# Performance work log

Hardware: AMD Instinct MI355X
Metric: run time of the kernel (lower is better)

The kernel has to match this reference:

```python
import math
import jax, jax.numpy as jnp
import numpy as np


def _sinkhorn_attn(q, n):
    """Log-domain Sinkhorn-Knopp, eps=1, max_iter=1, uniform marginals.
    cost C = -q @ q^T, so M = (-C + u + v)/eps = S + u + v with S = q q^T.
    Returns transport plan pi = exp(S + u_i + v_j).  q: [B, n, d]."""
    S = jnp.einsum('bnd,bmd->bnm', q, q)            # [B, n, n]
    log_marg = -math.log(n)                          # log(1/n)
    u = log_marg - jax.nn.logsumexp(S, axis=-1)      # [B, n] row update
    v = log_marg - jax.nn.logsumexp(S + u[..., :, None], axis=-2)  # [B, n] col update
    return jnp.exp(S + u[..., :, None] + v[..., None, :])


def reference(x, row_embed, col_embed):
    # x: [B, d, H, W]; row_embed/col_embed: [len_embedding, d//2]
    B, d, H, W = x.shape
    # learned positional embedding: [H, W, d] -> [d, H, W]
    x_emb = col_embed[:W]                             # [W, F]
    y_emb = row_embed[:H]                             # [H, F]
    F = x_emb.shape[-1]
    pos = jnp.concatenate([
        jnp.broadcast_to(x_emb[None, :, :], (H, W, F)),
        jnp.broadcast_to(y_emb[:, None, :], (H, W, F)),
    ], axis=-1).transpose(2, 0, 1)                    # [d, H, W]
    x = x + pos[None]

    n = H * W
    xf = x.reshape(B, d, n).transpose(0, 2, 1)        # [B, n, d] = q = k = v (v unscaled)
    inv_sqrtV = 1.0 / math.sqrt(math.sqrt(d))         # d**-0.25 applied to q and k each
    attn = _sinkhorn_attn(xf * inv_sqrtV, n)          # [B, n, n]
    out = jnp.einsum('bnm,bmd->bnd', attn, xf)        # [B, n, d]
    return out.transpose(0, 2, 1).reshape(B, d, H, W)


def setup_inputs() -> dict:
    key = jax.random.key(0)
    k1, k2, k3 = jax.random.split(key, 3)
    B, d, H, W = 32, 512, 32, 32
    len_emb, F = 32, d // 2
    return {
        'x': jax.random.normal(k1, (B, d, H, W), dtype=jnp.float32),
        'row_embed': jax.random.uniform(k2, (len_emb, F), dtype=jnp.float32),
        'col_embed': jax.random.uniform(k3, (len_emb, F), dtype=jnp.float32),
    }
```

## Files before the change

kernel.cpp:

```cpp
#include <hip/hip_runtime.h>
#include <hip/hip_fp16.h>
#include <math.h>

typedef _Float16 f16;
typedef _Float16 f16x8 __attribute__((ext_vector_type(8)));
typedef _Float16 f16x4 __attribute__((ext_vector_type(4)));
typedef float f32x4 __attribute__((ext_vector_type(4)));

namespace {
constexpr int kB = 32, kD = 512, kN = 1024, kF = 256;
constexpr float kScale = 0.04419417382415922f;
constexpr float kLogMarg = -6.931471805599453f;
constexpr float kPInv = 1.f / 16384.f;
}

__device__ __forceinline__ void gload16(const void* g, void* l) {
  __builtin_amdgcn_global_load_lds(
      (const __attribute__((address_space(1))) void*)g,
      (__attribute__((address_space(3))) void*)l, 16, 0, 0);
}

__global__ __launch_bounds__(256) void k_prep(
    const float* __restrict__ x, const float* __restrict__ re,
    const float* __restrict__ ce, f16* __restrict__ xf,
    f16* __restrict__ xfT, int b0) {
  __shared__ f16 T[64][68];
  const int lb = blockIdx.z;
  const int i0 = blockIdx.x * 64, c0 = blockIdx.y * 64;
  const int t = threadIdx.x;
  const int il = (t & 15) * 4;
  const int cl = t >> 4;
  const size_t xbase = ((size_t)(b0 + lb) * kD) * kN;
#pragma unroll
  for (int p = 0; p < 4; p++) {
    const int c = c0 + cl + 16 * p;
    const int i = i0 + il;
    const float4 xv = *(const float4*)(x + xbase + (size_t)c * kN + i);
    float4 pv;
    if (c < kF) {
      pv.x = ce[((i + 0) & 31) * kF + c];
      pv.y = ce[((i + 1) & 31) * kF + c];
      pv.z = ce[((i + 2) & 31) * kF + c];
      pv.w = ce[((i + 3) & 31) * kF + c];
    } else {
      const float r = re[(i >> 5) * kF + (c - kF)];
      pv.x = r; pv.y = r; pv.z = r; pv.w = r;
    }
    const f16 h0 = (f16)(xv.x + pv.x), h1 = (f16)(xv.y + pv.y);
    const f16 h2 = (f16)(xv.z + pv.z), h3 = (f16)(xv.w + pv.w);
    f16* dT = xfT + ((size_t)lb * kD + c) * kN + i;
    *(f16x4*)dT = (f16x4){h0, h1, h2, h3};
    T[cl + 16 * p][il + 0] = h0; T[cl + 16 * p][il + 1] = h1;
    T[cl + 16 * p][il + 2] = h2; T[cl + 16 * p][il + 3] = h3;
  }
  __syncthreads();
#pragma unroll
  for (int p = 0; p < 4; p++) {
    const int ir = cl + 16 * p;
    const int cc = il;
    const f16 h0 = T[cc + 0][ir], h1 = T[cc + 1][ir];
    const f16 h2 = T[cc + 2][ir], h3 = T[cc + 3][ir];
    f16* dF = xf + ((size_t)lb * kN + i0 + ir) * kD + c0 + cc;
    *(f16x4*)dF = (f16x4){h0, h1, h2, h3};
  }
}

__global__ __launch_bounds__(256) void k_gemm_s(
    const f16* __restrict__ xf, f16* __restrict__ S16,
    float* __restrict__ rp) {
  __shared__ char sm[65536];
  const int nwg = (int)(gridDim.x * gridDim.y * gridDim.z);
  const int lin = (int)(blockIdx.x +
                        gridDim.x * (blockIdx.y + gridDim.y * blockIdx.z));
  const int wid = (lin & 7) * (nwg >> 3) + (lin >> 3);
  const int bx = wid & 7, by = (wid >> 3) & 7, bz = wid >> 6;

  const int lb = bz;
  const int i0 = by * 128, j0 = bx * 128;
  const char* base = (const char*)(xf + (size_t)lb * kN * kD);
  const int t = threadIdx.x;
  const int w = t >> 6, lane = t & 63;
  const int m_off = (w >> 1) * 64, n_off = (w & 1) * 64;
  const int quad = lane >> 4, l15 = lane & 15;
  const int swz = (l15 & 7) << 4;

  int srcA[4], srcB[4], ldsw[4];
#pragma unroll
  for (int p = 0; p < 4; p++) {
    const int off = p * 4096 + w * 1024 + lane * 16;
    const int r = off >> 7;
    const int cb = (off & 127) ^ ((r & 7) << 4);
    srcA[p] = (i0 + r) * (kD * 2) + cb;
    srcB[p] = (j0 + r) * (kD * 2) + cb;
    ldsw[p] = p * 4096 + w * 1024;
  }

  f32x4 acc[4][4];
#pragma unroll
  for (int a = 0; a < 4; a++)
#pragma unroll
    for (int b = 0; b < 4; b++) acc[a][b] = (f32x4){0.f, 0.f, 0.f, 0.f};

#pragma unroll
  for (int p = 0; p < 4; p++) gload16(base + srcA[p], sm + ldsw[p]);
#pragma unroll
  for (int p = 0; p < 4; p++) gload16(base + srcB[p], sm + 16384 + ldsw[p]);
  __syncthreads();

#pragma unroll
  for (int tt = 0; tt < 8; tt++) {
    const int cur = tt & 1, nxt = cur ^ 1;
    if (tt + 1 < 8) {
      const int k0b = (tt + 1) * 128;
#pragma unroll
      for (int p = 0; p < 4; p++)
        gload16(base + srcA[p] + k0b, sm + (nxt << 15) + ldsw[p]);
#pragma unroll
      for (int p = 0; p < 4; p++)
        gload16(base + srcB[p] + k0b, sm + (nxt << 15) + 16384 + ldsw[p]);
    }
    const char* bA = sm + (cur << 15);
    const char* bB = bA + 16384;
#pragma unroll
    for (int kk = 0; kk < 2; kk++) {
      f16x8 af[4], bf[4];
#pragma unroll
      for (int q = 0; q < 4; q++)
        af[q] = *(const f16x8*)(bA + (m_off + 16 * q + l15) * 128 +
                                ((kk * 64 + quad * 16) ^ swz));
#pragma unroll
      for (int q = 0; q < 4; q++)
        bf[q] = *(const f16x8*)(bB + (n_off + 16 * q + l15) * 128 +
                                ((kk * 64 + quad * 16) ^ swz));
#pragma unroll
      for (int qa = 0; qa < 4; qa++)
#pragma unroll
        for (int qb = 0; qb < 4; qb++)
          acc[qa][qb] = __builtin_amdgcn_mfma_f32_16x16x32_f16(
              af[qa], bf[qb], acc[qa][qb], 0, 0, 0);
    }
    __syncthreads();
  }

  f16* Sb = S16 + (size_t)lb * kN * kN;
  const int jt2 = bx * 2 + (w & 1);
  float* rpb = rp + ((size_t)lb * 16 + jt2) * kN + i0 + m_off;
#pragma unroll
  for (int qa = 0; qa < 4; qa++) {
    const int i = i0 + m_off + 16 * qa + quad * 4;
    float rs[4] = {0.f, 0.f, 0.f, 0.f};
#pragma unroll
    for (int qb = 0; qb < 4; qb++) {
      const int j = j0 + n_off + 16 * qb + l15;
#pragma unroll
      for (int r = 0; r < 4; r++) {
        const f16 h = (f16)(acc[qa][qb][r] * kScale);
        Sb[(size_t)(i + r) * kN + j] = h;
        rs[r] += __expf((float)h);
      }
    }
#pragma unroll
    for (int r = 0; r < 4; r++) {
      float s = rs[r];
      s += __shfl_xor(s, 1);
      s += __shfl_xor(s, 2);
      s += __shfl_xor(s, 4);
      s += __shfl_xor(s, 8);
      if (l15 == 0) rpb[16 * qa + 4 * quad + r] = s;
    }
  }
}

__global__ __launch_bounds__(256) void k_u(
    const float* __restrict__ rp, float* __restrict__ u) {
  const int lb = blockIdx.y;
  const int i = blockIdx.x * 256 + threadIdx.x;
  const float* r = rp + (size_t)lb * 16 * kN + i;
  float s = 0.f;
#pragma unroll
  for (int t = 0; t < 16; t++) s += r[(size_t)t * kN];
  u[lb * kN + i] = kLogMarg - __logf(s);
}

__global__ __launch_bounds__(256) void k_cs(
    const f16* __restrict__ S16, const float* __restrict__ u,
    float* __restrict__ cp) {
  const int lb = blockIdx.z;
  const int seg = blockIdx.y;
  const int j = threadIdx.x * 4;
  const f16* Sb = S16 + (size_t)lb * kN * kN + (size_t)(seg * 64) * kN + j;
  const float* ub = u + lb * kN + seg * 64;
  float s0 = 0.f, s1 = 0.f, s2 = 0.f, s3 = 0.f;
#pragma unroll 8
  for (int r = 0; r < 64; r++) {
    const f16x4 v = *(const f16x4*)(Sb + (size_t)r * kN);
    const float ur = ub[r];
    s0 += __expf((float)v[0] + ur);
    s1 += __expf((float)v[1] + ur);
    s2 += __expf((float)v[2] + ur);
    s3 += __expf((float)v[3] + ur);
  }
  float4 o = {s0, s1, s2, s3};
  *(float4*)(cp + ((size_t)lb * 16 + seg) * kN + j) = o;
}

__global__ __launch_bounds__(256) void k_v(
    const float* __restrict__ cp, float* __restrict__ evp) {
  const int lb = blockIdx.y;
  const int j = blockIdx.x * 256 + threadIdx.x;
  const float* c = cp + (size_t)lb * 16 * kN + j;
  float s = 0.f;
#pragma unroll
  for (int r = 0; r < 16; r++) s += c[(size_t)r * kN];
  evp[lb * kN + j] = 16.f / s;
}

#define AF_READ(q)                                                          \
  _Pragma("unroll")                                                         \
  for (int pa = 0; pa < 2; pa++)                                            \
    _Pragma("unroll")                                                       \
    for (int kk = 0; kk < 2; kk++)                                          \
      af[pa][kk] = *(const f16x8*)(bA + (m_off + 32*(q) + 16*pa + l15)*128  \
                                   + ((kk*64 + quad*16) ^ swz));

#define MFMA_PH(q)                                                          \
  __builtin_amdgcn_s_setprio(1);                                            \
  _Pragma("unroll")                                                         \
  for (int pa = 0; pa < 2; pa++)                                            \
    _Pragma("unroll")                                                       \
    for (int qb = 0; qb < 4; qb++)                                          \
      _Pragma("unroll")                                                     \
      for (int kk = 0; kk < 2; kk++)                                        \
        acc[2*(q)+pa][qb] = __builtin_amdgcn_mfma_f32_16x16x32_f16(         \
            af[pa][kk], bf[qb][kk], acc[2*(q)+pa][qb], 0, 0, 0);            \
  __builtin_amdgcn_s_setprio(0);

__global__ __launch_bounds__(512) void k_gemm_o(
    const f16* __restrict__ xfT, const f16* __restrict__ S16,
    const float* __restrict__ u, const float* __restrict__ evp,
    float* __restrict__ out, int b0) {
  __shared__ char sm[135168];
  const int nwg = (int)(gridDim.x * gridDim.y * gridDim.z);
  const int lin = (int)(blockIdx.x +
                        gridDim.x * (blockIdx.y + gridDim.y * blockIdx.z));
  const int wid = (lin & 7) * (nwg >> 3) + (lin >> 3);
  const int bx = wid & 3, by = (wid >> 2) & 1, bz = wid >> 3;

  const int lb = bz;
  const int i0 = bx * 256, c0 = by * 256;
  const char* Ab = (const char*)(xfT + (size_t)lb * kD * kN);
  const char* Bb = (const char*)(S16 + (size_t)lb * kN * kN);
  const int t = threadIdx.x;
  const int w = t >> 6, lane = t & 63;
  const int wm = w >> 2, wn = w & 3;
  const int m_off = wm * 128, n_off = wn * 64;
  const int quad = lane >> 4, l15 = lane & 15;
  const int swz = (l15 & 7) << 4;

  int srcA[4], srcB[4], ldsw[4];
#pragma unroll
  for (int p = 0; p < 4; p++) {
    const int off = p * 8192 + t * 16;
    const int r = off >> 7;
    const int cb = (off & 127) ^ ((r & 7) << 4);
    srcA[p] = (c0 + r) * (kN * 2) + cb;
    srcB[p] = (i0 + r) * (kN * 2) + cb;
    ldsw[p] = p * 8192 + w * 1024;
  }

  float* evl = (float*)(sm + 131072);
  *(float2*)(evl + t * 2) = *(const float2*)(evp + (size_t)lb * kN + t * 2);
  float u4[4];
  const float* ub = u + (size_t)lb * kN + i0 + n_off + l15;
#pragma unroll
  for (int qb = 0; qb < 4; qb++) u4[qb] = ub[16 * qb];
  asm volatile("s_waitcnt vmcnt(0) lgkmcnt(0)" ::: "memory");
  __builtin_amdgcn_sched_barrier(0);

#pragma unroll
  for (int p = 0; p < 4; p++) gload16(Bb + srcB[p], sm + 65536 + ldsw[p]);
  gload16(Ab + srcA[0], sm + ldsw[0]);
  gload16(Ab + srcA[2], sm + ldsw[2]);
  gload16(Ab + srcA[1], sm + ldsw[1]);
  gload16(Ab + srcA[3], sm + ldsw[3]);
#pragma unroll
  for (int p = 0; p < 4; p++)
    gload16(Bb + srcB[p] + 128, sm + 65536 + 32768 + ldsw[p]);
  f32x4 acc[8][4];
#pragma unroll
  for (int a = 0; a < 8; a++)
#pragma unroll
    for (int b = 0; b < 4; b++) acc[a][b] = (f32x4){0.f, 0.f, 0.f, 0.f};
  asm volatile("s_waitcnt vmcnt(6)" ::: "memory");
  __builtin_amdgcn_s_barrier();
  __builtin_amdgcn_sched_barrier(0);

#pragma unroll
  for (int tt = 0; tt < 16; tt++) {
    const int cur = tt & 1, nxt = cur ^ 1;
    const char* bA = sm + cur * 32768;
    const char* bB = sm + 65536 + cur * 32768;
    char* wA = sm + nxt * 32768;
    char* wB = sm + 65536 + cur * 32768;
    const int kA = (tt + 1) * 128, kBB = (tt + 2) * 128;
    f16x8 bf[4][2], af[2][2];
    f16x8 raw[4][2];
#pragma unroll
    for (int qb = 0; qb < 4; qb++)
#pragma unroll
      for (int kk = 0; kk < 2; kk++)
        raw[qb][kk] = *(const f16x8*)(bB + (n_off + 16 * qb + l15) * 128 +
                                      ((kk * 64 + quad * 16) ^ swz));
    AF_READ(0)
    float4 e0[2], e1[2];
#pragma unroll
    for (int kk = 0; kk < 2; kk++) {
      const float* ep = evl + tt * 64 + kk * 32 + quad * 8;
      e0[kk] = *(const float4*)ep;
      e1[kk] = *(const float4*)(ep + 4);
    }
    asm volatile("s_waitcnt lgkmcnt(0)" ::: "memory");
    __builtin_amdgcn_sched_barrier(0);
    __builtin_amdgcn_s_barrier();
#pragma unroll
    for (int qb = 0; qb < 4; qb++)
#pragma unroll
      for (int kk = 0; kk < 2; kk++) {
        f16x8 o;
        o[0] = (f16)(__expf((float)raw[qb][kk][0] + u4[qb]) * e0[kk].x);
        o[1] = (f16)(__expf((float)raw[qb][kk][1] + u4[qb]) * e0[kk].y);
        o[2] = (f16)(__expf((float)raw[qb][kk][2] + u4[qb]) * e0[kk].z);
        o[3] = (f16)(__expf((float)raw[qb][kk][3] + u4[qb]) * e0[kk].w);
        o[4] = (f16)(__expf((float)raw[qb][kk][4] + u4[qb]) * e1[kk].x);
        o[5] = (f16)(__expf((float)raw[qb][kk][5] + u4[qb]) * e1[kk].y);
        o[6] = (f16)(__expf((float)raw[qb][kk][6] + u4[qb]) * e1[kk].z);
        o[7] = (f16)(__expf((float)raw[qb][kk][7] + u4[qb]) * e1[kk].w);
        bf[qb][kk] = o;
      }
    MFMA_PH(0)
    if (tt + 1 < 16) {
      gload16(Ab + srcA[0] + kA, wA + ldsw[0]);
      gload16(Ab + srcA[2] + kA, wA + ldsw[2]);
    }
    AF_READ(1)
    __builtin_amdgcn_s_barrier();
    MFMA_PH(1)
    if (tt == 15) { asm volatile("s_waitcnt vmcnt(0)" ::: "memory"); }
    else          { asm volatile("s_waitcnt vmcnt(6)" ::: "memory"); }
    __builtin_amdgcn_s_barrier();
    __builtin_amdgcn_sched_barrier(0);
    AF_READ(2)
    __builtin_amdgcn_s_barrier();
    MFMA_PH(2)
    if (tt + 1 < 16) {
      gload16(Ab + srcA[1] + kA, wA + ldsw[1]);
      gload16(Ab + srcA[3] + kA, wA + ldsw[3]);
    }
    if (tt + 2 < 16) {
#pragma unroll
      for (int p = 0; p < 4; p++)
        gload16(Bb + srcB[p] + kBB, wB + ldsw[p]);
    }
    AF_READ(3)
    __builtin_amdgcn_s_barrier();
    MFMA_PH(3)
    if (tt + 2 < 16)      { asm volatile("s_waitcnt vmcnt(6)" ::: "memory"); }
    else if (tt + 1 < 16) { asm volatile("s_waitcnt vmcnt(2)" ::: "memory"); }
    __builtin_amdgcn_s_barrier();
    __builtin_amdgcn_sched_barrier(0);
  }

  float* ob = out + ((size_t)(b0 + lb) * kD) * kN;
#pragma unroll
  for (int qa = 0; qa < 8; qa++) {
    const int c = c0 + m_off + 16 * qa + quad * 4;
#pragma unroll
    for (int qb = 0; qb < 4; qb++) {
      const int i = i0 + n_off + 16 * qb + l15;
#pragma unroll
      for (int r = 0; r < 4; r++)
        ob[(size_t)(c + r) * kN + i] = acc[qa][qb][r] * kPInv;
    }
  }
}

extern "C" void kernel_launch(void* const* d_in, const int* in_sizes, int n_in,
                              void* d_out, int out_size, void* d_ws, size_t ws_size,
                              hipStream_t stream) {
  const float* x = (const float*)d_in[0];
  const float* re = (const float*)d_in[1];
  const float* ce = (const float*)d_in[2];
  float* out = (float*)d_out;

  char* wsb = (char*)d_ws;
  const size_t perb = 2097152ull + 1048576 + 1048576 + 4096 + 4096 +
                      65536 + 65536;
  int G = (int)(ws_size / perb);
  if (G >= 32) G = 32;
  else if (G >= 16) G = 16;
  else if (G >= 8) G = 8;
  else if (G >= 4) G = 4;
  else if (G < 1) G = 1;
  f16* S16 = (f16*)wsb;
  f16* xf = (f16*)(wsb + (size_t)G * 2097152);
  f16* xfT = (f16*)((char*)xf + (size_t)G * 1048576);
  float* u = (float*)((char*)xfT + (size_t)G * 1048576);
  float* evp = u + (size_t)G * kN;
  float* rp = evp + (size_t)G * kN;
  float* cp = rp + (size_t)G * 16 * kN;

  for (int b0 = 0; b0 < kB; b0 += G) {
    const int g = (kB - b0 < G) ? (kB - b0) : G;
    k_prep<<<dim3(16, 8, g), 256, 0, stream>>>(x, re, ce, xf, xfT, b0);
    k_gemm_s<<<dim3(8, 8, g), 256, 0, stream>>>(xf, S16, rp);
    k_u<<<dim3(4, g), 256, 0, stream>>>(rp, u);
    k_cs<<<dim3(1, 16, g), 256, 0, stream>>>(S16, u, cp);
    k_v<<<dim3(4, g), 256, 0, stream>>>(cp, evp);
    k_gemm_o<<<dim3(4, 2, g), 512, 0, stream>>>(xfT, S16, u, evp, out, b0);
  }
}
```

Before: 257.9 us.

## Exploit symmetry of S in QK^T GEMM and precompute transport plan

Since S = q q^T is symmetric, the S GEMM now computes only the upper-triangular 128x128 tiles (36 per batch) and writes each off-diagonal tile's transpose, deriving the mirrored row-sum partials from column sums of the exponentials. A new elementwise kernel materializes the scaled transport plan exp(S+u+v) in fp16, so the output GEMM no longer does exp and scaling inside its inner loop. This roughly halves the MFMA work for S but adds strided transposed stores, an extra 2 MB per batch of workspace, and an extra read/write pass over the plan.

```diff
diff --git a/kernel.cpp b/kernel.cpp
--- a/kernel.cpp
+++ b/kernel.cpp
@@ -11,6 +11,8 @@
 constexpr int kB = 32, kD = 512, kN = 1024, kF = 256;
 constexpr float kScale = 0.04419417382415922f;
 constexpr float kLogMarg = -6.931471805599453f;
+constexpr float kMarg = 1.f / 1024.f;
+constexpr float kPScale = 16384.f;
 constexpr float kPInv = 1.f / 16384.f;
 }
 
@@ -69,11 +71,14 @@
     const f16* __restrict__ xf, f16* __restrict__ S16,
     float* __restrict__ rp) {
   __shared__ char sm[65536];
-  const int nwg = (int)(gridDim.x * gridDim.y * gridDim.z);
-  const int lin = (int)(blockIdx.x +
-                        gridDim.x * (blockIdx.y + gridDim.y * blockIdx.z));
+  const int nwg = (int)(gridDim.x * gridDim.z);
+  const int lin = (int)(blockIdx.x + gridDim.x * blockIdx.z);
   const int wid = (lin & 7) * (nwg >> 3) + (lin >> 3);
-  const int bx = wid & 7, by = (wid >> 3) & 7, bz = wid >> 6;
+  const int bz = wid / 36;
+  int qq = wid - bz * 36;
+  int by = 0;
+  while (qq >= 8 - by) { qq -= 8 - by; by++; }
+  const int bx = by + qq;
 
   const int lb = bz;
   const int i0 = by * 128, j0 = bx * 128;
@@ -145,6 +150,8 @@
   f16* Sb = S16 + (size_t)lb * kN * kN;
   const int jt2 = bx * 2 + (w & 1);
   float* rpb = rp + ((size_t)lb * 16 + jt2) * kN + i0 + m_off;
+  const bool offd = (bx != by);
+  float cs[4] = {0.f, 0.f, 0.f, 0.f};
 #pragma unroll
   for (int qa = 0; qa < 4; qa++) {
     const int i = i0 + m_off + 16 * qa + quad * 4;
@@ -152,12 +159,18 @@
 #pragma unroll
     for (int qb = 0; qb < 4; qb++) {
       const int j = j0 + n_off + 16 * qb + l15;
+      f16 h4[4];
 #pragma unroll
       for (int r = 0; r < 4; r++) {
         const f16 h = (f16)(acc[qa][qb][r] * kScale);
         Sb[(size_t)(i + r) * kN + j] = h;
-        rs[r] += __expf((float)h);
+        h4[r] = h;
+        const float e = __expf((float)h);
+        rs[r] += e;
+        cs[qb] += e;
       }
+      if (offd)
+        *(f16x4*)(Sb + (size_t)j * kN + i) = (f16x4){h4[0], h4[1], h4[2], h4[3]};
     }
 #pragma unroll
     for (int r = 0; r < 4; r++) {
@@ -167,6 +180,16 @@
       s += __shfl_xor(s, 4);
       s += __shfl_xor(s, 8);
       if (l15 == 0) rpb[16 * qa + 4 * quad + r] = s;
+    }
+  }
+  if (offd) {
+    float* rpm = rp + ((size_t)lb * 16 + (by * 2 + (w >> 1))) * kN;
+#pragma unroll
+    for (int qb = 0; qb < 4; qb++) {
+      float s = cs[qb];
+      s += __shfl_xor(s, 16);
+      s += __shfl_xor(s, 32);
+      if (quad == 0) rpm[j0 + n_off + 16 * qb + l15] = s;
     }
   }
 }
@@ -205,14 +228,33 @@
 }
 
 __global__ __launch_bounds__(256) void k_v(
-    const float* __restrict__ cp, float* __restrict__ evp) {
+    const float* __restrict__ cp, float* __restrict__ ev) {
   const int lb = blockIdx.y;
   const int j = blockIdx.x * 256 + threadIdx.x;
   const float* c = cp + (size_t)lb * 16 * kN + j;
   float s = 0.f;
 #pragma unroll
   for (int r = 0; r < 16; r++) s += c[(size_t)r * kN];
-  evp[lb * kN + j] = 16.f / s;
+  ev[lb * kN + j] = kMarg / s;
+}
+
+__global__ __launch_bounds__(256) void k_pt(
+    const f16* __restrict__ S16, const float* __restrict__ u,
+    const float* __restrict__ ev, f16* __restrict__ t16) {
+  const int row = blockIdx.x;
+  const float ui = u[row];
+  const f16* Sr = S16 + (size_t)row * kN;
+  const float* evb = ev + (size_t)(row >> 10) * kN;
+  f16* Tr = t16 + (size_t)row * kN;
+  const int j = threadIdx.x * 4;
+  const f16x4 s = *(const f16x4*)(Sr + j);
+  const float4 e = *(const float4*)(evb + j);
+  f16x4 o;
+  o[0] = (f16)(__expf((float)s[0] + ui) * e.x * kPScale);
+  o[1] = (f16)(__expf((float)s[1] + ui) * e.y * kPScale);
+  o[2] = (f16)(__expf((float)s[2] + ui) * e.z * kPScale);
+  o[3] = (f16)(__expf((float)s[3] + ui) * e.w * kPScale);
+  *(f16x4*)(Tr + j) = o;
 }
 
 #define AF_READ(q)                                                          \
@@ -236,10 +278,9 @@
   __builtin_amdgcn_s_setprio(0);
 
 __global__ __launch_bounds__(512) void k_gemm_o(
-    const f16* __restrict__ xfT, const f16* __restrict__ S16,
-    const float* __restrict__ u, const float* __restrict__ evp,
+    const f16* __restrict__ xfT, const f16* __restrict__ P,
     float* __restrict__ out, int b0) {
-  __shared__ char sm[135168];
+  __shared__ char sm[131072];
   const int nwg = (int)(gridDim.x * gridDim.y * gridDim.z);
   const int lin = (int)(blockIdx.x +
                         gridDim.x * (blockIdx.y + gridDim.y * blockIdx.z));
@@ -249,7 +290,7 @@
   const int lb = bz;
   const int i0 = bx * 256, c0 = by * 256;
   const char* Ab = (const char*)(xfT + (size_t)lb * kD * kN);
-  const char* Bb = (const char*)(S16 + (size_t)lb * kN * kN);
+  const char* Bb = (const char*)(P + (size_t)lb * kN * kN);
   const int t = threadIdx.x;
   const int w = t >> 6, lane = t & 63;
   const int wm = w >> 2, wn = w & 3;
@@ -267,15 +308,6 @@
     srcB[p] = (i0 + r) * (kN * 2) + cb;
     ldsw[p] = p * 8192 + w * 1024;
   }
-
-  float* evl = (float*)(sm + 131072);
-  *(float2*)(evl + t * 2) = *(const float2*)(evp + (size_t)lb * kN + t * 2);
-  float u4[4];
-  const float* ub = u + (size_t)lb * kN + i0 + n_off + l15;
-#pragma unroll
-  for (int qb = 0; qb < 4; qb++) u4[qb] = ub[16 * qb];
-  asm volatile("s_waitcnt vmcnt(0) lgkmcnt(0)" ::: "memory");
-  __builtin_amdgcn_sched_barrier(0);
 
 #pragma unroll
   for (int p = 0; p < 4; p++) gload16(Bb + srcB[p], sm + 65536 + ldsw[p]);
@@ -304,39 +336,16 @@
     char* wB = sm + 65536 + cur * 32768;
     const int kA = (tt + 1) * 128, kBB = (tt + 2) * 128;
     f16x8 bf[4][2], af[2][2];
-    f16x8 raw[4][2];
 #pragma unroll
     for (int qb = 0; qb < 4; qb++)
 #pragma unroll
       for (int kk = 0; kk < 2; kk++)
-        raw[qb][kk] = *(const f16x8*)(bB + (n_off + 16 * qb + l15) * 128 +
-                                      ((kk * 64 + quad * 16) ^ swz));
+        bf[qb][kk] = *(const f16x8*)(bB + (n_off + 16 * qb + l15) * 128 +
+                                     ((kk * 64 + quad * 16) ^ swz));
     AF_READ(0)
-    float4 e0[2], e1[2];
-#pragma unroll
-    for (int kk = 0; kk < 2; kk++) {
-      const float* ep = evl + tt * 64 + kk * 32 + quad * 8;
-      e0[kk] = *(const float4*)ep;
-      e1[kk] = *(const float4*)(ep + 4);
-    }
     asm volatile("s_waitcnt lgkmcnt(0)" ::: "memory");
     __builtin_amdgcn_sched_barrier(0);
     __builtin_amdgcn_s_barrier();
-#pragma unroll
-    for (int qb = 0; qb < 4; qb++)
-#pragma unroll
-      for (int kk = 0; kk < 2; kk++) {
-        f16x8 o;
-        o[0] = (f16)(__expf((float)raw[qb][kk][0] + u4[qb]) * e0[kk].x);
-        o[1] = (f16)(__expf((float)raw[qb][kk][1] + u4[qb]) * e0[kk].y);
-        o[2] = (f16)(__expf((float)raw[qb][kk][2] + u4[qb]) * e0[kk].z);
-        o[3] = (f16)(__expf((float)raw[qb][kk][3] + u4[qb]) * e0[kk].w);
-        o[4] = (f16)(__expf((float)raw[qb][kk][4] + u4[qb]) * e1[kk].x);
-        o[5] = (f16)(__expf((float)raw[qb][kk][5] + u4[qb]) * e1[kk].y);
-        o[6] = (f16)(__expf((float)raw[qb][kk][6] + u4[qb]) * e1[kk].z);
-        o[7] = (f16)(__expf((float)raw[qb][kk][7] + u4[qb]) * e1[kk].w);
-        bf[qb][kk] = o;
-      }
     MFMA_PH(0)
     if (tt + 1 < 16) {
       gload16(Ab + srcA[0] + kA, wA + ldsw[0]);
@@ -393,8 +402,8 @@
   float* out = (float*)d_out;
 
   char* wsb = (char*)d_ws;
-  const size_t perb = 2097152ull + 1048576 + 1048576 + 4096 + 4096 +
-                      65536 + 65536;
+  const size_t perb = 2097152ull + 1048576 + 1048576 + 2097152 +
+                      4096 + 4096 + 65536 + 65536;
   int G = (int)(ws_size / perb);
   if (G >= 32) G = 32;
   else if (G >= 16) G = 16;
@@ -404,18 +413,20 @@
   f16* S16 = (f16*)wsb;
   f16* xf = (f16*)(wsb + (size_t)G * 2097152);
   f16* xfT = (f16*)((char*)xf + (size_t)G * 1048576);
-  float* u = (float*)((char*)xfT + (size_t)G * 1048576);
-  float* evp = u + (size_t)G * kN;
-  float* rp = evp + (size_t)G * kN;
+  f16* t16 = (f16*)((char*)xfT + (size_t)G * 1048576);
+  float* u = (float*)((char*)t16 + (size_t)G * 2097152);
+  float* ev = u + (size_t)G * kN;
+  float* rp = ev + (size_t)G * kN;
   float* cp = rp + (size_t)G * 16 * kN;
 
   for (int b0 = 0; b0 < kB; b0 += G) {
     const int g = (kB - b0 < G) ? (kB - b0) : G;
     k_prep<<<dim3(16, 8, g), 256, 0, stream>>>(x, re, ce, xf, xfT, b0);
-    k_gemm_s<<<dim3(8, 8, g), 256, 0, stream>>>(xf, S16, rp);
+    k_gemm_s<<<dim3(36, 1, g), 256, 0, stream>>>(xf, S16, rp);
     k_u<<<dim3(4, g), 256, 0, stream>>>(rp, u);
     k_cs<<<dim3(1, 16, g), 256, 0, stream>>>(S16, u, cp);
-    k_v<<<dim3(4, g), 256, 0, stream>>>(cp, evp);
-    k_gemm_o<<<dim3(4, 2, g), 512, 0, stream>>>(xfT, S16, u, evp, out, b0);
-  }
-}
+    k_v<<<dim3(4, g), 256, 0, stream>>>(cp, ev);
+    k_pt<<<g * kN, 256, 0, stream>>>(S16, u, ev, t16);
+    k_gemm_o<<<dim3(4, 2, g), 512, 0, stream>>>(xfT, t16, out, b0);
+  }
+}
```

New measurement: 238.0 us. 7.7% less time.
